# Performance work log

Measured on AMD Instinct MI355X. Metric: run time of the kernel, lower is better.

The kernel has to match this reference:

```python
import jax, jax.numpy as jnp
import numpy as np

K = 2  # kernel_size == stride (required by the module's output view)


def setup_inputs() -> dict:
    key = jax.random.key(0)
    k1, k2, k3, k4, k5 = jax.random.split(key, 5)
    b, c, h, w = 16, 64, 224, 224
    x = jax.random.normal(k1, (b, c, h, w), dtype=jnp.float32)
    # torch nn.Linear params: W1 [16, K*K], b1 [16], W2 [1, 16], b2 [1]
    s1 = 1.0 / np.sqrt(K * K)
    s2 = 1.0 / np.sqrt(16)
    W1 = jax.random.uniform(k2, (16, K * K), jnp.float32, -s1, s1)
    b1 = jax.random.uniform(k3, (16,), jnp.float32, -s1, s1)
    W2 = jax.random.uniform(k4, (1, 16), jnp.float32, -s2, s2)
    b2 = jax.random.uniform(k5, (1,), jnp.float32, -s2, s2)
    return {"x": x, "W1": W1, "b1": b1, "W2": W2, "b2": b2}


def reference(x, W1, b1, W2, b2):
    b, c, h, w = x.shape
    nh, nw = h // K, w // K
    # non-overlapping KxK patches, flattened row-major within patch
    # (matches torch unfold(2,K,K).unfold(3,K,K).view(..., K*K))
    patches = x.reshape(b, c, nh, K, nw, K)
    patches = patches.transpose(0, 1, 2, 4, 3, 5).reshape(b, c, nh, nw, K * K)
    # tiny MLP per patch: K*K -> 16 -> 1
    hdn = jax.nn.relu(jnp.einsum('bcijk,hk->bcijh', patches, W1) + b1)
    out = jnp.einsum('bcijh,oh->bcijo', hdn, W2) + b2
    return out[..., 0]  # [b, c, h//K, w//K]
```

## Files before the change

kernel.cpp:

```cpp
#include <hip/hip_runtime.h>


#define NH 112
#define NW 112
#define GPR 28

__global__ __launch_bounds__(256)
void nn_pool_kernel(const float* __restrict__ x,
                    const float* __restrict__ W1,
                    const float* __restrict__ b1,
                    const float* __restrict__ W2,
                    const float* __restrict__ b2,
                    float* __restrict__ out,
                    int n_groups)
{
    float w10[16], w11[16], w12[16], w13[16], bb1[16], w2[16];
#pragma unroll
    for (int h = 0; h < 16; ++h) {
        w10[h] = W1[4 * h + 0];
        w11[h] = W1[4 * h + 1];
        w12[h] = W1[4 * h + 2];
        w13[h] = W1[4 * h + 3];
        bb1[h] = b1[h];
        w2[h]  = W2[h];
    }
    const float bias2 = b2[0];

    const int stride = gridDim.x * blockDim.x;
    for (int g = blockIdx.x * blockDim.x + threadIdx.x; g < n_groups; g += stride) {
        const int jg = g % GPR;
        const int t  = g / GPR;
        const int i  = t % NH;
        const int bc = t / NH;

        const float* row0 = x + (size_t)bc * (224 * 224) + (size_t)(2 * i) * 224 + 8 * jg;
        const float* row1 = row0 + 224;

        const float4 r0a = *reinterpret_cast<const float4*>(row0);
        const float4 r0b = *reinterpret_cast<const float4*>(row0 + 4);
        const float4 r1a = *reinterpret_cast<const float4*>(row1);
        const float4 r1b = *reinterpret_cast<const float4*>(row1 + 4);

        const float p0x = r0a.x, p0y = r0a.y, p0z = r1a.x, p0w = r1a.y;
        const float p1x = r0a.z, p1y = r0a.w, p1z = r1a.z, p1w = r1a.w;
        const float p2x = r0b.x, p2y = r0b.y, p2z = r1b.x, p2w = r1b.y;
        const float p3x = r0b.z, p3y = r0b.w, p3z = r1b.z, p3w = r1b.w;

        float a0 = bias2, a1 = bias2, a2 = bias2, a3 = bias2;
#pragma unroll
        for (int h = 0; h < 16; ++h) {
            float s0 = fmaf(w10[h], p0x, bb1[h]);
            float s1 = fmaf(w10[h], p1x, bb1[h]);
            float s2 = fmaf(w10[h], p2x, bb1[h]);
            float s3 = fmaf(w10[h], p3x, bb1[h]);
            s0 = fmaf(w11[h], p0y, s0);
            s1 = fmaf(w11[h], p1y, s1);
            s2 = fmaf(w11[h], p2y, s2);
            s3 = fmaf(w11[h], p3y, s3);
            s0 = fmaf(w12[h], p0z, s0);
            s1 = fmaf(w12[h], p1z, s1);
            s2 = fmaf(w12[h], p2z, s2);
            s3 = fmaf(w12[h], p3z, s3);
            s0 = fmaf(w13[h], p0w, s0);
            s1 = fmaf(w13[h], p1w, s1);
            s2 = fmaf(w13[h], p2w, s2);
            s3 = fmaf(w13[h], p3w, s3);
            a0 = fmaf(w2[h], fmaxf(s0, 0.0f), a0);
            a1 = fmaf(w2[h], fmaxf(s1, 0.0f), a1);
            a2 = fmaf(w2[h], fmaxf(s2, 0.0f), a2);
            a3 = fmaf(w2[h], fmaxf(s3, 0.0f), a3);
        }

        float4 res;
        res.x = a0; res.y = a1; res.z = a2; res.w = a3;
        *reinterpret_cast<float4*>(out + (size_t)bc * (NH * NW) + (size_t)i * NW + 4 * jg) = res;
    }
}

extern "C" void kernel_launch(void* const* d_in, const int* in_sizes, int n_in,
                              void* d_out, int out_size, void* d_ws, size_t ws_size,
                              hipStream_t stream) {
    const float* x  = (const float*)d_in[0];
    const float* W1 = (const float*)d_in[1];
    const float* b1 = (const float*)d_in[2];
    const float* W2 = (const float*)d_in[3];
    const float* b2 = (const float*)d_in[4];
    float* out = (float*)d_out;

    const int n_groups = out_size / 4;
    const int block = 256;
    const int grid = 2048;
    nn_pool_kernel<<<grid, block, 0, stream>>>(x, W1, b1, W2, b2, out, n_groups);
}
```

Before: 300.2 us.

## Use one-shot grid with two patches per thread instead of grid-stride loop

Replaces the persistent grid-stride loop (2048 blocks, four patches per thread) with a full grid where each thread handles two adjacent 2x2 patches, loading two float4s and storing a float2. Index math is simplified by treating (b,c,i) as one flattened row index. The intent is more memory parallelism and less per-thread work so the bandwidth-bound kernel keeps more loads in flight. The costs are more blocks, each thread reloading the weights, and narrower float2 stores.

```diff
diff --git a/kernel.cpp b/kernel.cpp
--- a/kernel.cpp
+++ b/kernel.cpp
@@ -1,9 +1,7 @@
 #include <hip/hip_runtime.h>
 
 
-#define NH 112
-#define NW 112
-#define GPR 28
+#define NJ 56
 
 __global__ __launch_bounds__(256)
 void nn_pool_kernel(const float* __restrict__ x,
@@ -12,69 +10,49 @@
                     const float* __restrict__ W2,
                     const float* __restrict__ b2,
                     float* __restrict__ out,
-                    int n_groups)
+                    int n_units)
 {
-    float w10[16], w11[16], w12[16], w13[16], bb1[16], w2[16];
+    const int tid = blockIdx.x * 256 + threadIdx.x;
+    if (tid >= n_units) return;
+
+    const int j = tid % NJ;
+    const int r = tid / NJ;
+
+    const float* p0 = x + (size_t)r * 448 + j * 4;
+    const float4 t0 = *reinterpret_cast<const float4*>(p0);
+    const float4 t1 = *reinterpret_cast<const float4*>(p0 + 224);
+
+    float w0[16], w1[16], w2c[16], w3[16], bb[16], v2[16];
 #pragma unroll
     for (int h = 0; h < 16; ++h) {
-        w10[h] = W1[4 * h + 0];
-        w11[h] = W1[4 * h + 1];
-        w12[h] = W1[4 * h + 2];
-        w13[h] = W1[4 * h + 3];
-        bb1[h] = b1[h];
-        w2[h]  = W2[h];
+        w0[h]  = W1[4 * h + 0];
+        w1[h]  = W1[4 * h + 1];
+        w2c[h] = W1[4 * h + 2];
+        w3[h]  = W1[4 * h + 3];
+        bb[h]  = b1[h];
+        v2[h]  = W2[h];
     }
-    const float bias2 = b2[0];
+    const float c2 = b2[0];
 
-    const int stride = gridDim.x * blockDim.x;
-    for (int g = blockIdx.x * blockDim.x + threadIdx.x; g < n_groups; g += stride) {
-        const int jg = g % GPR;
-        const int t  = g / GPR;
-        const int i  = t % NH;
-        const int bc = t / NH;
+    float aA = c2, aB = c2;
+#pragma unroll
+    for (int h = 0; h < 16; ++h) {
+        float sA = fmaf(w0[h], t0.x, bb[h]);
+        float sB = fmaf(w0[h], t0.z, bb[h]);
+        sA = fmaf(w1[h], t0.y, sA);
+        sB = fmaf(w1[h], t0.w, sB);
+        sA = fmaf(w2c[h], t1.x, sA);
+        sB = fmaf(w2c[h], t1.z, sB);
+        sA = fmaf(w3[h], t1.y, sA);
+        sB = fmaf(w3[h], t1.w, sB);
+        aA = fmaf(v2[h], fmaxf(sA, 0.0f), aA);
+        aB = fmaf(v2[h], fmaxf(sB, 0.0f), aB);
+    }
 
-        const float* row0 = x + (size_t)bc * (224 * 224) + (size_t)(2 * i) * 224 + 8 * jg;
-        const float* row1 = row0 + 224;
-
-        const float4 r0a = *reinterpret_cast<const float4*>(row0);
-        const float4 r0b = *reinterpret_cast<const float4*>(row0 + 4);
-        const float4 r1a = *reinterpret_cast<const float4*>(row1);
-        const float4 r1b = *reinterpret_cast<const float4*>(row1 + 4);
-
-        const float p0x = r0a.x, p0y = r0a.y, p0z = r1a.x, p0w = r1a.y;
-        const float p1x = r0a.z, p1y = r0a.w, p1z = r1a.z, p1w = r1a.w;
-        const float p2x = r0b.x, p2y = r0b.y, p2z = r1b.x, p2w = r1b.y;
-        const float p3x = r0b.z, p3y = r0b.w, p3z = r1b.z, p3w = r1b.w;
-
-        float a0 = bias2, a1 = bias2, a2 = bias2, a3 = bias2;
-#pragma unroll
-        for (int h = 0; h < 16; ++h) {
-            float s0 = fmaf(w10[h], p0x, bb1[h]);
-            float s1 = fmaf(w10[h], p1x, bb1[h]);
-            float s2 = fmaf(w10[h], p2x, bb1[h]);
-            float s3 = fmaf(w10[h], p3x, bb1[h]);
-            s0 = fmaf(w11[h], p0y, s0);
-            s1 = fmaf(w11[h], p1y, s1);
-            s2 = fmaf(w11[h], p2y, s2);
-            s3 = fmaf(w11[h], p3y, s3);
-            s0 = fmaf(w12[h], p0z, s0);
-            s1 = fmaf(w12[h], p1z, s1);
-            s2 = fmaf(w12[h], p2z, s2);
-            s3 = fmaf(w12[h], p3z, s3);
-            s0 = fmaf(w13[h], p0w, s0);
-            s1 = fmaf(w13[h], p1w, s1);
-            s2 = fmaf(w13[h], p2w, s2);
-            s3 = fmaf(w13[h], p3w, s3);
-            a0 = fmaf(w2[h], fmaxf(s0, 0.0f), a0);
-            a1 = fmaf(w2[h], fmaxf(s1, 0.0f), a1);
-            a2 = fmaf(w2[h], fmaxf(s2, 0.0f), a2);
-            a3 = fmaf(w2[h], fmaxf(s3, 0.0f), a3);
-        }
-
-        float4 res;
-        res.x = a0; res.y = a1; res.z = a2; res.w = a3;
-        *reinterpret_cast<float4*>(out + (size_t)bc * (NH * NW) + (size_t)i * NW + 4 * jg) = res;
-    }
+    float2 res;
+    res.x = aA;
+    res.y = aB;
+    *reinterpret_cast<float2*>(out + (size_t)r * 112 + j * 2) = res;
 }
 
 extern "C" void kernel_launch(void* const* d_in, const int* in_sizes, int n_in,
@@ -87,8 +65,8 @@
     const float* b2 = (const float*)d_in[4];
     float* out = (float*)d_out;
 
-    const int n_groups = out_size / 4;
+    const int n_units = out_size / 2;
     const int block = 256;
-    const int grid = 2048;
-    nn_pool_kernel<<<grid, block, 0, stream>>>(x, W1, b1, W2, b2, out, n_groups);
+    const int grid = (n_units + block - 1) / block;
+    nn_pool_kernel<<<grid, block, 0, stream>>>(x, W1, b1, W2, b2, out, n_units);
 }
```

Measured after the change: 290.4 us. 1.03x faster.
